# Kernel optimization log

Hardware: AMD Instinct MI355X
Metric: run time of the kernel (lower is better)

The kernel has to match this reference:

```python
import math
import jax, jax.numpy as jnp
import numpy as np


def setup_inputs() -> dict:
    key = jax.random.key(0)
    k1, k2 = jax.random.split(key)
    x = jax.random.normal(k1, (16, 256, 4096), dtype=jnp.float32)          # [B, D, T]
    codebooks = jax.random.normal(k2, (8, 1024, 256), dtype=jnp.float32)   # [n_q, bins, D]
    return {"x": x, "codebooks": codebooks, "sample_rate": 24000}


def _rvq(xt, codebooks):
    """Residual VQ on channels-last input xt: [B, T, D]. codebooks: [n_q, bins, D]."""
    n_q = codebooks.shape[0]
    residual = xt
    quant_out = jnp.zeros_like(xt)
    codes = []
    losses = []
    for i in range(n_q):
        cb = codebooks[i]                                   # [bins, D]
        # squared euclidean distance: ||r||^2 - 2 r.e + ||e||^2  -> [B, T, bins]
        dist = (jnp.sum(residual * residual, axis=-1, keepdims=True)
                - 2.0 * jnp.einsum("btd,kd->btk", residual, cb)
                + jnp.sum(cb * cb, axis=-1))
        idx = jnp.argmin(dist, axis=-1)                     # [B, T]
        q = cb[idx]                                         # gather -> [B, T, D]
        # straight-through estimator
        q_st = residual + jax.lax.stop_gradient(q - residual)
        # commitment loss: mse(stop_grad(quantize), residual)
        losses.append(jnp.mean((jax.lax.stop_gradient(q_st) - residual) ** 2))
        residual = residual - q_st
        quant_out = quant_out + q_st
        codes.append(idx)
    codes = jnp.stack(codes)                                # [n_q, B, T]
    commit_loss = jnp.stack(losses)                         # [n_q]
    return quant_out, codes, commit_loss


def reference(x, codebooks, sample_rate):
    n_q, bins, _ = codebooks.shape
    bw_per_q = math.log2(bins) * sample_rate / 1000.0
    xt = jnp.transpose(x, (0, 2, 1))                        # [B, T, D]
    quant_out, codes, commit_loss = _rvq(xt, codebooks)
    quantized = jnp.transpose(quant_out, (0, 2, 1))         # [B, D, T]
    bw = jnp.asarray(n_q * bw_per_q, dtype=x.dtype)
    return quantized, codes, bw, jnp.mean(commit_loss)
```

## Files before the change

### kernel.cpp

```cpp
#include <hip/hip_runtime.h>

#define B 16
#define D 256
#define T 4096
#define NQ 8
#define BINS 1024
#define EPS 0.008f

#define OFF_C  ((size_t)B * D * T)
#define OFF_BW (OFF_C + (size_t)NQ * B * T)
#define OFF_L  (OFF_BW + 1)

typedef __attribute__((ext_vector_type(8))) short short8v;
typedef __attribute__((ext_vector_type(4))) float float4v;

#define BBUF   0
#define RESF   0
#define IDXS   32768
#define FLAGS  33024
#define G1L    33280
#define RSTG   33536
#define NORMS  34560
#define REDW   38656
#define REDIW  38688
#define SMTOT  38704

#define STAGE16(gp, loff) \
  __builtin_amdgcn_global_load_lds( \
      (const __attribute__((address_space(1))) unsigned int*)(gp), \
      (__attribute__((address_space(3))) unsigned int*)(smc + (loff)), 16, 0, 0)

__device__ __forceinline__ unsigned short f2bf(float f) {
    unsigned u = __float_as_uint(f);
    unsigned r = (u + 0x7fffu + ((u >> 16) & 1u)) >> 16;
    return (unsigned short)r;
}
__device__ __forceinline__ float bf2f(unsigned short h) {
    return __uint_as_float(((unsigned)h) << 16);
}

__global__ __launch_bounds__(256) void cbnorm_kernel(const float* __restrict__ cb,
                                                     double* __restrict__ cbn,
                                                     float* __restrict__ cbnf)
{
    const int wave = threadIdx.x >> 6;
    const int lane = threadIdx.x & 63;
    const int bin = blockIdx.x * 4 + wave;
    const float4 v = *(const float4*)&cb[(size_t)bin * D + lane * 4];
    double a = (double)v.x * v.x + (double)v.y * v.y
             + (double)v.z * v.z + (double)v.w * v.w;
    #pragma unroll
    for (int off = 32; off >= 1; off >>= 1)
        a += __shfl_xor(a, off, 64);
    if (lane == 0) { cbn[bin] = a; cbnf[bin] = (float)a; }
}

__global__ __launch_bounds__(256) void prep_bfrag(const float* __restrict__ cb,
                                                  unsigned short* __restrict__ bfh,
                                                  unsigned short* __restrict__ bfl)
{
    const int c = blockIdx.x * 4 + (threadIdx.x >> 6);
    const int lane = threadIdx.x & 63;
    const int q = c >> 9, ntg = (c >> 3) & 63, ks = c & 7;
    const float* src = cb + ((size_t)q * BINS + ntg * 16 + (lane & 15)) * D
                         + ks * 32 + (lane >> 4) * 8;
    short8v h, l;
    #pragma unroll
    for (int j = 0; j < 8; ++j) {
        const float v = src[j];
        const unsigned short hh = f2bf(v);
        h[j] = (short)hh;
        l[j] = (short)f2bf(v - bf2f(hh));
    }
    const size_t off = ((size_t)c * 64 + lane) * 8;
    *(short8v*)(bfh + off) = h;
    *(short8v*)(bfl + off) = l;
}

__global__ __launch_bounds__(256, 4) void rvq_scan(
    const float* __restrict__ rsrc, float* __restrict__ rdst,
    const float* __restrict__ cb,
    const double* __restrict__ cbn, const float* __restrict__ cbnf,
    const unsigned short* __restrict__ bfh, const unsigned short* __restrict__ bfl,
    float* __restrict__ out, double* __restrict__ lpart, int q)
{
    __shared__ __align__(16) char smem[SMTOT];
    char*   smc    = smem;
    float*  resf   = (float*)(smem + RESF);
    int*    idxsL  = (int*)(smem + IDXS);
    int*    flagsL = (int*)(smem + FLAGS);
    float*  g1L    = (float*)(smem + G1L);
    float*  rstage = (float*)(smem + RSTG);
    float*  normsp = (float*)(smem + NORMS);
    double* redw   = (double*)(smem + REDW);
    int*    rediw  = (int*)(smem + REDIW);

    const int tid  = threadIdx.x;
    const int bid  = blockIdx.x;
    const int b    = bid >> 6;
    const int t0   = (bid & 63) * 64;
    const int w    = tid >> 6;
    const int lane = tid & 63;
    const int col  = lane & 15;
    const int rgrp = lane >> 4;
    const int rot  = (bid * 5) & 63;

    const float* rs = rsrc + (size_t)b * D * T + t0;
    float*       rd = rdst + (size_t)b * D * T + t0;

    for (int i = tid; i < BINS; i += 256) normsp[i] = cbnf[q * BINS + i];

    short8v Ah[8], Al[8];
    #pragma unroll 1
    for (int ch = 0; ch < 4; ++ch) {
        #pragma unroll 1
        for (int it = 0; it < 16; ++it) {
            const int lin = it * 256 + tid;
            const int tk = lin & 15, d = lin >> 4;
            resf[tk * 257 + d] = rs[(size_t)d * T + ch * 16 + tk];
        }
        __syncthreads();
        if (w == ch) {
            #pragma unroll
            for (int ks = 0; ks < 8; ++ks) {
                short8v h, l;
                #pragma unroll
                for (int j = 0; j < 8; ++j) {
                    const float v = resf[col * 257 + ks * 32 + rgrp * 8 + j];
                    const unsigned short hh = f2bf(v);
                    h[j] = (short)hh;
                    l[j] = (short)f2bf(v - bf2f(hh));
                }
                Ah[ks] = h; Al[ks] = l;
            }
        }
        __syncthreads();
    }

    const int plane = w >> 1, part = w & 1;
    const unsigned short* sbase = plane ? bfl : bfh;

    {
        const unsigned short* srcp =
            sbase + ((size_t)q * 512 + rot * 8 + part * 4) * 512 + lane * 8;
        const int dstb = plane * 8192 + part * 4096;
        #pragma unroll
        for (int i = 0; i < 4; ++i) STAGE16(srcp + i * 512, dstb + i * 1024);
    }

    float bv1[4], bv2[4]; int bi1[4];
    #pragma unroll
    for (int s = 0; s < 4; ++s) { bv1[s] = 3.4e38f; bv2[s] = 3.4e38f; bi1[s] = 0; }

    #pragma unroll 1
    for (int nt = 0; nt < 64; ++nt) {
        asm volatile("s_waitcnt vmcnt(0)" ::: "memory");
        __builtin_amdgcn_s_barrier();
        asm volatile("" ::: "memory");

        const int cur = nt & 1;
        if (nt < 63) {
            const int ntg = (nt + 1 + rot) & 63;
            const unsigned short* srcp =
                sbase + ((size_t)q * 512 + ntg * 8 + part * 4) * 512 + lane * 8;
            const int dstb = (cur ^ 1) * 16384 + plane * 8192 + part * 4096;
            #pragma unroll
            for (int i = 0; i < 4; ++i) STAGE16(srcp + i * 512, dstb + i * 1024);
        }
        asm volatile("" ::: "memory");

        const int ntr = (nt + rot) & 63;
        const char* bb = smc + cur * 16384;
        const float qn = normsp[ntr * 16 + col];

        float4v a0 = {0,0,0,0}, a1 = {0,0,0,0}, a2 = {0,0,0,0}, a3 = {0,0,0,0};
        __builtin_amdgcn_s_setprio(1);
        #pragma unroll
        for (int ks = 0; ks < 8; ++ks) {
            const short8v Bh = *(const short8v*)(bb + ks * 1024 + lane * 16);
            const short8v Bl = *(const short8v*)(bb + 8192 + ks * 1024 + lane * 16);
            float4v& c = (ks & 3) == 0 ? a0 : ((ks & 3) == 1 ? a1 : ((ks & 3) == 2 ? a2 : a3));
            c = __builtin_amdgcn_mfma_f32_16x16x32_bf16(Al[ks], Bh, c, 0, 0, 0);
            c = __builtin_amdgcn_mfma_f32_16x16x32_bf16(Ah[ks], Bl, c, 0, 0, 0);
            c = __builtin_amdgcn_mfma_f32_16x16x32_bf16(Ah[ks], Bh, c, 0, 0, 0);
        }
        __builtin_amdgcn_s_setprio(0);

        const int binb = ntr * 16 + col;
        #pragma unroll
        for (int r = 0; r < 4; ++r) {
            const float s0 = fmaf(-2.0f, (a0[r] + a1[r]) + (a2[r] + a3[r]), qn);
            if (s0 < bv1[r]) { bv2[r] = bv1[r]; bv1[r] = s0; bi1[r] = binb; }
            else if (s0 < bv2[r]) bv2[r] = s0;
        }
    }

    #pragma unroll
    for (int off = 1; off <= 8; off <<= 1) {
        #pragma unroll
        for (int sl = 0; sl < 4; ++sl) {
            const float ov1 = __shfl_xor(bv1[sl], off, 64);
            const float ov2 = __shfl_xor(bv2[sl], off, 64);
            const int   oi  = __shfl_xor(bi1[sl], off, 64);
            if (ov1 < bv1[sl] || (ov1 == bv1[sl] && oi < bi1[sl])) {
                bv2[sl] = fminf(bv1[sl], ov2); bv1[sl] = ov1; bi1[sl] = oi;
            } else {
                bv2[sl] = fminf(bv2[sl], ov1);
            }
        }
    }
    if (col == 0) {
        #pragma unroll
        for (int r = 0; r < 4; ++r) {
            const int tk = w * 16 + rgrp * 4 + r;
            idxsL[tk]  = bi1[r];
            g1L[tk]    = bv1[r];
            flagsL[tk] = (bv2[r] - bv1[r] < EPS) ? 1 : 0;
        }
    }
    __syncthreads();

    const float* cbq = cb + (size_t)q * BINS * D;
    #pragma unroll 1
    for (int tk2 = 0; tk2 < 64; ++tk2) {
        if (!flagsL[tk2]) continue;
        rstage[tid] = rs[(size_t)tid * T + tk2];
        __syncthreads();
        const float thr = g1L[tk2] + 0.0065f;
        double bb2 = 1e300; int bbi = 0x7fffffff;
        #pragma unroll 1
        for (int jj = 0; jj < 4; ++jj) {
            const int bin = tid + 256 * jj;
            const float* crow = cbq + (size_t)bin * D;
            float f0 = 0.f, f1 = 0.f, f2 = 0.f, f3 = 0.f;
            for (int d = 0; d < D; d += 4) {
                const float4 rv = *(const float4*)&rstage[d];
                const float4 cv = *(const float4*)&crow[d];
                f0 = fmaf(rv.x, cv.x, f0); f1 = fmaf(rv.y, cv.y, f1);
                f2 = fmaf(rv.z, cv.z, f2); f3 = fmaf(rv.w, cv.w, f3);
            }
            const float sf = fmaf(-2.0f, (f0 + f1) + (f2 + f3), normsp[bin]);
            if (sf <= thr) {
                double a = 0.0;
                for (int d = 0; d < D; d += 4) {
                    const float4 rv = *(const float4*)&rstage[d];
                    const float4 cv = *(const float4*)&crow[d];
                    a = fma((double)rv.x, (double)cv.x, a);
                    a = fma((double)rv.y, (double)cv.y, a);
                    a = fma((double)rv.z, (double)cv.z, a);
                    a = fma((double)rv.w, (double)cv.w, a);
                }
                const double s = fma(-2.0, a, cbn[q * BINS + bin]);
                if (s < bb2) { bb2 = s; bbi = bin; }
            }
        }
        #pragma unroll
        for (int off = 32; off >= 1; off >>= 1) {
            const double ov = __shfl_xor(bb2, off, 64);
            const int   oi  = __shfl_xor(bbi, off, 64);
            if (ov < bb2 || (ov == bb2 && oi < bbi)) { bb2 = ov; bbi = oi; }
        }
        if (lane == 0) { redw[w] = bb2; rediw[w] = bbi; }
        __syncthreads();
        if (tid == 0) {
            double mv = redw[0]; int mi = rediw[0];
            #pragma unroll
            for (int wv = 1; wv < 4; ++wv) {
                const double ov = redw[wv]; const int oi = rediw[wv];
                if (ov < mv || (ov == mv && oi < mi)) { mv = ov; mi = oi; }
            }
            idxsL[tk2] = mi;
        }
        __syncthreads();
    }

    if (tid < 64)
        out[OFF_C + (size_t)q * B * T + (size_t)b * T + t0 + tid] = (float)idxsL[tid];

    float* rows = resf;
    double lacc = 0.0;
    #pragma unroll 1
    for (int g = 0; g < 4; ++g) {
        __syncthreads();
        {
            const int j = tid >> 4, c = tid & 15;
            const float* crow = cbq + (size_t)idxsL[g * 16 + j] * D + c * 16;
            #pragma unroll
            for (int k2 = 0; k2 < 4; ++k2) {
                const float4 v = *(const float4*)(crow + k2 * 4);
                *(float4*)&rows[j * 257 + c * 16 + k2 * 4] = v;
            }
        }
        __syncthreads();
        #pragma unroll
        for (int it = 0; it < 16; ++it) {
            const int tk16 = tid & 15;
            const int dd_  = it * 16 + (tid >> 4);
            const int tk   = g * 16 + tk16;
            const float r  = rs[(size_t)dd_ * T + tk];
            const float cv = rows[tk16 * 257 + dd_];
            const float e   = cv - r;
            const float qst = r + e;
            const float dv  = qst - r;
            lacc = fma((double)dv, (double)dv, lacc);
            rd[(size_t)dd_ * T + tk] = r - qst;
        }
    }

    #pragma unroll
    for (int off = 32; off >= 1; off >>= 1)
        lacc += __shfl_xor(lacc, off, 64);
    __syncthreads();
    if (lane == 0) redw[w] = lacc;
    __syncthreads();
    if (tid == 0)
        lpart[(size_t)q * 1024 + bid] = (redw[0] + redw[1]) + (redw[2] + redw[3]);
}

__global__ __launch_bounds__(256) void final_sub(const float* __restrict__ x,
                                                 float* __restrict__ o)
{
    const size_t i = ((size_t)blockIdx.x * 256 + threadIdx.x) * 4;
    const float4v xv = __builtin_nontemporal_load((const float4v*)(x + i));
    const float4v ov = __builtin_nontemporal_load((const float4v*)(o + i));
    const float4v r = xv - ov;
    __builtin_nontemporal_store(r, (float4v*)(o + i));
}

#define OTOK 32
#define ORS 260
__global__ __launch_bounds__(256, 3) void rvq_main_old(
    const float* __restrict__ x, const float* __restrict__ cb,
    const double* __restrict__ cbn, const float* __restrict__ cbnf,
    float* __restrict__ out, double* __restrict__ lpart)
{
    __shared__ float  res[OTOK][ORS];
    __shared__ float  bv1s[OTOK][16];
    __shared__ float  bv2s[OTOK][16];
    __shared__ int    bi1s[OTOK][16];
    __shared__ int    idxs[OTOK];
    __shared__ int    flags[OTOK];
    __shared__ double fbv[256];
    __shared__ int    fbi[256];

    const int tid = threadIdx.x;
    const int bid = blockIdx.x;
    const int b  = bid >> 7;
    const int t0 = (bid & 127) * OTOK;

    const float* xb = x + (size_t)b * D * T + t0;
    #pragma unroll
    for (int it = 0; it < 32; ++it) {
        const int d  = it * 8 + (tid >> 5);
        const int tk = tid & 31;
        res[tk][d] = xb[(size_t)d * T + tk];
    }
    __syncthreads();

    float qreg[32];
    #pragma unroll
    for (int i = 0; i < 32; ++i) qreg[i] = 0.0f;

    const int tg = tid & 15;
    const int bg = tid >> 4;
    const int tku = tid >> 3;
    const int d0u = (tid & 7) * 32;
    double lacc = 0.0;

    for (int q = 0; q < NQ; ++q) {
        const float*  cbq = cb   + (size_t)q * BINS * D;
        const float*  cnf = cbnf + (size_t)q * BINS;
        const double* cnd = cbn  + (size_t)q * BINS;

        float bvA = 3.4e38f, bvA2 = 3.4e38f;  int biA = 0;
        float bvB = 3.4e38f, bvB2 = 3.4e38f;  int biB = 0;

        for (int iter = 0; iter < 8; ++iter) {
            const int binbase = iter * 128 + bg * 8;
            float a0[8], a1[8];
            #pragma unroll
            for (int j = 0; j < 8; ++j) { a0[j] = 0.0f; a1[j] = 0.0f; }
            for (int d = 0; d < D; d += 4) {
                const float4 r0 = *(const float4*)&res[tg][d];
                const float4 r1 = *(const float4*)&res[tg + 16][d];
                #pragma unroll
                for (int j = 0; j < 8; ++j) {
                    const float4 c = *(const float4*)&cbq[(size_t)(binbase + j) * D + d];
                    a0[j] = fmaf(r0.x, c.x, a0[j]); a0[j] = fmaf(r0.y, c.y, a0[j]);
                    a0[j] = fmaf(r0.z, c.z, a0[j]); a0[j] = fmaf(r0.w, c.w, a0[j]);
                    a1[j] = fmaf(r1.x, c.x, a1[j]); a1[j] = fmaf(r1.y, c.y, a1[j]);
                    a1[j] = fmaf(r1.z, c.z, a1[j]); a1[j] = fmaf(r1.w, c.w, a1[j]);
                }
            }
            #pragma unroll
            for (int j = 0; j < 8; ++j) {
                const int bin = binbase + j;
                const float qn = cnf[bin];
                const float s0 = fmaf(-2.0f, a0[j], qn);
                const float s1 = fmaf(-2.0f, a1[j], qn);
                if (s0 < bvA) { bvA2 = bvA; bvA = s0; biA = bin; }
                else if (s0 < bvA2) { bvA2 = s0; }
                if (s1 < bvB) { bvB2 = bvB; bvB = s1; biB = bin; }
                else if (s1 < bvB2) { bvB2 = s1; }
            }
        }
        bv1s[tg][bg]      = bvA;  bv2s[tg][bg]      = bvA2;  bi1s[tg][bg]      = biA;
        bv1s[tg + 16][bg] = bvB;  bv2s[tg + 16][bg] = bvB2;  bi1s[tg + 16][bg] = biB;
        __syncthreads();

        if (tid < OTOK) {
            float g1 = bv1s[tid][0], g2 = bv2s[tid][0];
            int   gi = bi1s[tid][0];
            #pragma unroll
            for (int g = 1; g < 16; ++g) {
                const float v1 = bv1s[tid][g];
                const float v2 = bv2s[tid][g];
                const int   i1 = bi1s[tid][g];
                if (v1 < g1 || (v1 == g1 && i1 < gi)) { g2 = fminf(g1, v2); g1 = v1; gi = i1; }
                else g2 = fminf(g2, v1);
            }
            idxs[tid]  = gi;
            flags[tid] = (g2 - g1 < 0.02f) ? 1 : 0;
        }
        __syncthreads();

        for (int tok = 0; tok < OTOK; ++tok) {
            if (!flags[tok]) continue;
            double bb = 1e300; int bbi = 0;
            #pragma unroll
            for (int jj = 0; jj < 4; ++jj) {
                const int bin = tid + 256 * jj;
                const float* crow = cbq + (size_t)bin * D;
                double a = 0.0;
                for (int d = 0; d < D; d += 4) {
                    const float4 r = *(const float4*)&res[tok][d];
                    const float4 c = *(const float4*)&crow[d];
                    a = fma((double)r.x, (double)c.x, a);
                    a = fma((double)r.y, (double)c.y, a);
                    a = fma((double)r.z, (double)c.z, a);
                    a = fma((double)r.w, (double)c.w, a);
                }
                const double s = fma(-2.0, a, cnd[bin]);
                if (s < bb) { bb = s; bbi = bin; }
            }
            fbv[tid] = bb; fbi[tid] = bbi;
            __syncthreads();
            for (int s2 = 128; s2 >= 1; s2 >>= 1) {
                if (tid < s2) {
                    const double ov = fbv[tid + s2]; const int oi = fbi[tid + s2];
                    const double mv = fbv[tid];      const int mi = fbi[tid];
                    if (ov < mv || (ov == mv && oi < mi)) { fbv[tid] = ov; fbi[tid] = oi; }
                }
                __syncthreads();
            }
            if (tid == 0) idxs[tok] = fbi[0];
            __syncthreads();
        }

        if (tid < OTOK)
            out[OFF_C + (size_t)q * B * T + (size_t)b * T + t0 + tid] = (float)idxs[tid];

        const float* crow = cbq + (size_t)idxs[tku] * D;
        #pragma unroll
        for (int i = 0; i < 8; ++i) {
            const int d = d0u + i * 4;
            const float4 qv = *(const float4*)&crow[d];
            float4 r = *(float4*)&res[tku][d];
            float e, qst, dd;
            e = qv.x - r.x; qst = r.x + e; dd = qst - r.x;
            lacc = fma((double)dd, (double)dd, lacc); qreg[i*4+0] += qst; r.x = r.x - qst;
            e = qv.y - r.y; qst = r.y + e; dd = qst - r.y;
            lacc = fma((double)dd, (double)dd, lacc); qreg[i*4+1] += qst; r.y = r.y - qst;
            e = qv.z - r.z; qst = r.z + e; dd = qst - r.z;
            lacc = fma((double)dd, (double)dd, lacc); qreg[i*4+2] += qst; r.z = r.z - qst;
            e = qv.w - r.w; qst = r.w + e; dd = qst - r.w;
            lacc = fma((double)dd, (double)dd, lacc); qreg[i*4+3] += qst; r.w = r.w - qst;
            *(float4*)&res[tku][d] = r;
        }
        __syncthreads();
    }

    #pragma unroll
    for (int i = 0; i < 8; ++i)
        *(float4*)&res[tku][d0u + i * 4] = *(float4*)&qreg[i * 4];
    __syncthreads();
    #pragma unroll
    for (int it = 0; it < 32; ++it) {
        const int d  = it * 8 + (tid >> 5);
        const int tk = tid & 31;
        out[(size_t)b * D * T + (size_t)d * T + t0 + tk] = res[tk][d];
    }

    fbv[tid] = lacc;
    __syncthreads();
    for (int s2 = 128; s2 >= 1; s2 >>= 1) {
        if (tid < s2) fbv[tid] += fbv[tid + s2];
        __syncthreads();
    }
    if (tid == 0) lpart[bid] = fbv[0];
}

__global__ __launch_bounds__(256) void finalize_kernel(
    const double* __restrict__ lpart, int nblk,
    const int* __restrict__ srp, float* __restrict__ out)
{
    __shared__ double sh[256];
    double a = 0.0;
    for (int i = threadIdx.x; i < nblk; i += 256) a += lpart[i];
    sh[threadIdx.x] = a;
    __syncthreads();
    for (int s = 128; s >= 1; s >>= 1) {
        if (threadIdx.x < s) sh[threadIdx.x] += sh[threadIdx.x + s];
        __syncthreads();
    }
    if (threadIdx.x == 0) {
        out[OFF_L]  = (float)(sh[0] / ((double)NQ * B * T * D));
        out[OFF_BW] = (float)((double)NQ * 10.0 * (double)srp[0] / 1000.0);
    }
}

extern "C" void kernel_launch(void* const* d_in, const int* in_sizes, int n_in,
                              void* d_out, int out_size, void* d_ws, size_t ws_size,
                              hipStream_t stream)
{
    const float* x  = (const float*)d_in[0];
    const float* cb = (const float*)d_in[1];
    const int*   sr = (const int*)d_in[2];
    float* out = (float*)d_out;

    double* cbn   = (double*)d_ws;
    float*  cbnf  = (float*)((char*)d_ws + 65536);
    double* lpart = (double*)((char*)d_ws + 98304);
    unsigned short* bfh = (unsigned short*)((char*)d_ws + 163840);
    unsigned short* bfl = (unsigned short*)((char*)d_ws + 4358144);

    hipLaunchKernelGGL(cbnorm_kernel, dim3(NQ * BINS / 4), dim3(256), 0, stream, cb, cbn, cbnf);

    if (ws_size >= (size_t)8552448) {
        hipLaunchKernelGGL(prep_bfrag, dim3(1024), dim3(256), 0, stream, cb, bfh, bfl);
        float* resb = out;
        for (int q = 0; q < NQ; ++q) {
            hipLaunchKernelGGL(rvq_scan, dim3(B * (T / 64)), dim3(256), 0, stream,
                               (q == 0 ? x : (const float*)resb), resb, cb, cbn, cbnf,
                               bfh, bfl, out, lpart, q);
        }
        hipLaunchKernelGGL(final_sub, dim3((B * D * T) / 1024), dim3(256), 0, stream, x, resb);
        hipLaunchKernelGGL(finalize_kernel, dim3(1), dim3(256), 0, stream,
                           lpart, NQ * 1024, sr, out);
    } else {
        hipLaunchKernelGGL(rvq_main_old, dim3(B * (T / OTOK)), dim3(256), 0, stream,
                           x, cb, cbn, cbnf, out, lpart);
        hipLaunchKernelGGL(finalize_kernel, dim3(1), dim3(256), 0, stream,
                           lpart, B * (T / OTOK), sr, out);
    }
}
```

Measured before the change: 1.652 ms.

## Split codebook across wave pairs and give each wave two row tiles

Each wave now holds the bf16 hi/lo fragments for two 16-row tiles of residual vectors and scans only half of the codebook bins. Two waves sharing a row group split the bins between them, and their top-two candidates are merged through shared memory afterwards. Every codebook fragment read from LDS now feeds twice as many MFMAs, which halves the LDS reads per MFMA and halves the scan loop trip count. In exchange the kernel uses more registers and doubles the LDS staging buffer, so launch bounds drop to 2 blocks per CU and occupancy falls.

```diff
diff --git a/kernel.cpp b/kernel.cpp
--- a/kernel.cpp
+++ b/kernel.cpp
@@ -16,14 +16,17 @@
 
 #define BBUF   0
 #define RESF   0
-#define IDXS   32768
-#define FLAGS  33024
-#define G1L    33280
-#define RSTG   33536
-#define NORMS  34560
-#define REDW   38656
-#define REDIW  38688
-#define SMTOT  38704
+#define NORMS  65536
+#define MG1    69632
+#define MG2    70144
+#define MGI    70656
+#define IDXS   71168
+#define FLAGS  71424
+#define G1L    71680
+#define RSTG   71936
+#define REDW   72960
+#define REDIW  72992
+#define SMTOT  73008
 
 #define STAGE16(gp, loff) \
   __builtin_amdgcn_global_load_lds( \
@@ -77,7 +80,7 @@
     *(short8v*)(bfl + off) = l;
 }
 
-__global__ __launch_bounds__(256, 4) void rvq_scan(
+__global__ __launch_bounds__(256, 2) void rvq_scan(
     const float* __restrict__ rsrc, float* __restrict__ rdst,
     const float* __restrict__ cb,
     const double* __restrict__ cbn, const float* __restrict__ cbnf,
@@ -87,11 +90,14 @@
     __shared__ __align__(16) char smem[SMTOT];
     char*   smc    = smem;
     float*  resf   = (float*)(smem + RESF);
+    float*  normsp = (float*)(smem + NORMS);
+    float*  mg1    = (float*)(smem + MG1);
+    float*  mg2    = (float*)(smem + MG2);
+    int*    mgi    = (int*)(smem + MGI);
     int*    idxsL  = (int*)(smem + IDXS);
     int*    flagsL = (int*)(smem + FLAGS);
     float*  g1L    = (float*)(smem + G1L);
     float*  rstage = (float*)(smem + RSTG);
-    float*  normsp = (float*)(smem + NORMS);
     double* redw   = (double*)(smem + REDW);
     int*    rediw  = (int*)(smem + REDIW);
 
@@ -103,14 +109,16 @@
     const int lane = tid & 63;
     const int col  = lane & 15;
     const int rgrp = lane >> 4;
-    const int rot  = (bid * 5) & 63;
+    const int tg   = w >> 1;
+    const int bh   = w & 1;
+    const int rot  = (bid * 5) & 31;
 
     const float* rs = rsrc + (size_t)b * D * T + t0;
     float*       rd = rdst + (size_t)b * D * T + t0;
 
     for (int i = tid; i < BINS; i += 256) normsp[i] = cbnf[q * BINS + i];
 
-    short8v Ah[8], Al[8];
+    short8v Ah0[8], Al0[8], Ah1[8], Al1[8];
     #pragma unroll 1
     for (int ch = 0; ch < 4; ++ch) {
         #pragma unroll 1
@@ -120,7 +128,8 @@
             resf[tk * 257 + d] = rs[(size_t)d * T + ch * 16 + tk];
         }
         __syncthreads();
-        if (w == ch) {
+        if ((ch >> 1) == tg) {
+            const int mt = ch & 1;
             #pragma unroll
             for (int ks = 0; ks < 8; ++ks) {
                 short8v h, l;
@@ -131,74 +140,83 @@
                     h[j] = (short)hh;
                     l[j] = (short)f2bf(v - bf2f(hh));
                 }
-                Ah[ks] = h; Al[ks] = l;
-            }
-        }
-        __syncthreads();
-    }
-
-    const int plane = w >> 1, part = w & 1;
-    const unsigned short* sbase = plane ? bfl : bfh;
+                if (mt == 0) { Ah0[ks] = h; Al0[ks] = l; }
+                else         { Ah1[ks] = h; Al1[ks] = l; }
+            }
+        }
+        __syncthreads();
+    }
+
+    const int sh = w & 1, sp = w >> 1;
+    const unsigned short* sbase = sp ? bfl : bfh;
 
     {
         const unsigned short* srcp =
-            sbase + ((size_t)q * 512 + rot * 8 + part * 4) * 512 + lane * 8;
-        const int dstb = plane * 8192 + part * 4096;
-        #pragma unroll
-        for (int i = 0; i < 4; ++i) STAGE16(srcp + i * 512, dstb + i * 1024);
-    }
-
-    float bv1[4], bv2[4]; int bi1[4];
-    #pragma unroll
-    for (int s = 0; s < 4; ++s) { bv1[s] = 3.4e38f; bv2[s] = 3.4e38f; bi1[s] = 0; }
+            sbase + ((size_t)q * 512 + (sh * 32 + rot) * 8) * 512 + lane * 8;
+        const int dstb = sh * 16384 + sp * 8192;
+        #pragma unroll
+        for (int i = 0; i < 8; ++i) STAGE16(srcp + i * 512, dstb + i * 1024);
+    }
+
+    float bv1[8], bv2[8]; int bi1[8];
+    #pragma unroll
+    for (int s = 0; s < 8; ++s) { bv1[s] = 3.4e38f; bv2[s] = 3.4e38f; bi1[s] = 0; }
 
     #pragma unroll 1
-    for (int nt = 0; nt < 64; ++nt) {
+    for (int nt = 0; nt < 32; ++nt) {
         asm volatile("s_waitcnt vmcnt(0)" ::: "memory");
         __builtin_amdgcn_s_barrier();
         asm volatile("" ::: "memory");
 
         const int cur = nt & 1;
-        if (nt < 63) {
-            const int ntg = (nt + 1 + rot) & 63;
+        if (nt < 31) {
+            const int ntg = (nt + 1 + rot) & 31;
             const unsigned short* srcp =
-                sbase + ((size_t)q * 512 + ntg * 8 + part * 4) * 512 + lane * 8;
-            const int dstb = (cur ^ 1) * 16384 + plane * 8192 + part * 4096;
-            #pragma unroll
-            for (int i = 0; i < 4; ++i) STAGE16(srcp + i * 512, dstb + i * 1024);
+                sbase + ((size_t)q * 512 + (sh * 32 + ntg) * 8) * 512 + lane * 8;
+            const int dstb = (cur ^ 1) * 32768 + sh * 16384 + sp * 8192;
+            #pragma unroll
+            for (int i = 0; i < 8; ++i) STAGE16(srcp + i * 512, dstb + i * 1024);
         }
         asm volatile("" ::: "memory");
 
-        const int ntr = (nt + rot) & 63;
-        const char* bb = smc + cur * 16384;
-        const float qn = normsp[ntr * 16 + col];
-
-        float4v a0 = {0,0,0,0}, a1 = {0,0,0,0}, a2 = {0,0,0,0}, a3 = {0,0,0,0};
+        const int ntr = (nt + rot) & 31;
+        const char* bbse = smc + cur * 32768 + bh * 16384;
+        const int binb = bh * 512 + ntr * 16 + col;
+        const float qn = normsp[binb];
+
+        float4v a00 = {0,0,0,0}, a01 = {0,0,0,0}, a02 = {0,0,0,0}, a03 = {0,0,0,0};
+        float4v a10 = {0,0,0,0}, a11 = {0,0,0,0}, a12 = {0,0,0,0}, a13 = {0,0,0,0};
         __builtin_amdgcn_s_setprio(1);
         #pragma unroll
         for (int ks = 0; ks < 8; ++ks) {
-            const short8v Bh = *(const short8v*)(bb + ks * 1024 + lane * 16);
-            const short8v Bl = *(const short8v*)(bb + 8192 + ks * 1024 + lane * 16);
-            float4v& c = (ks & 3) == 0 ? a0 : ((ks & 3) == 1 ? a1 : ((ks & 3) == 2 ? a2 : a3));
-            c = __builtin_amdgcn_mfma_f32_16x16x32_bf16(Al[ks], Bh, c, 0, 0, 0);
-            c = __builtin_amdgcn_mfma_f32_16x16x32_bf16(Ah[ks], Bl, c, 0, 0, 0);
-            c = __builtin_amdgcn_mfma_f32_16x16x32_bf16(Ah[ks], Bh, c, 0, 0, 0);
+            const short8v Bh = *(const short8v*)(bbse + ks * 1024 + lane * 16);
+            const short8v Bl = *(const short8v*)(bbse + 8192 + ks * 1024 + lane * 16);
+            float4v& c0 = (ks & 3) == 0 ? a00 : ((ks & 3) == 1 ? a01 : ((ks & 3) == 2 ? a02 : a03));
+            float4v& c1 = (ks & 3) == 0 ? a10 : ((ks & 3) == 1 ? a11 : ((ks & 3) == 2 ? a12 : a13));
+            c0 = __builtin_amdgcn_mfma_f32_16x16x32_bf16(Al0[ks], Bh, c0, 0, 0, 0);
+            c1 = __builtin_amdgcn_mfma_f32_16x16x32_bf16(Al1[ks], Bh, c1, 0, 0, 0);
+            c0 = __builtin_amdgcn_mfma_f32_16x16x32_bf16(Ah0[ks], Bl, c0, 0, 0, 0);
+            c1 = __builtin_amdgcn_mfma_f32_16x16x32_bf16(Ah1[ks], Bl, c1, 0, 0, 0);
+            c0 = __builtin_amdgcn_mfma_f32_16x16x32_bf16(Ah0[ks], Bh, c0, 0, 0, 0);
+            c1 = __builtin_amdgcn_mfma_f32_16x16x32_bf16(Ah1[ks], Bh, c1, 0, 0, 0);
         }
         __builtin_amdgcn_s_setprio(0);
 
-        const int binb = ntr * 16 + col;
         #pragma unroll
         for (int r = 0; r < 4; ++r) {
-            const float s0 = fmaf(-2.0f, (a0[r] + a1[r]) + (a2[r] + a3[r]), qn);
+            const float s0 = fmaf(-2.0f, (a00[r] + a01[r]) + (a02[r] + a03[r]), qn);
             if (s0 < bv1[r]) { bv2[r] = bv1[r]; bv1[r] = s0; bi1[r] = binb; }
             else if (s0 < bv2[r]) bv2[r] = s0;
+            const float s1 = fmaf(-2.0f, (a10[r] + a11[r]) + (a12[r] + a13[r]), qn);
+            if (s1 < bv1[4+r]) { bv2[4+r] = bv1[4+r]; bv1[4+r] = s1; bi1[4+r] = binb; }
+            else if (s1 < bv2[4+r]) bv2[4+r] = s1;
         }
     }
 
     #pragma unroll
     for (int off = 1; off <= 8; off <<= 1) {
         #pragma unroll
-        for (int sl = 0; sl < 4; ++sl) {
+        for (int sl = 0; sl < 8; ++sl) {
             const float ov1 = __shfl_xor(bv1[sl], off, 64);
             const float ov2 = __shfl_xor(bv2[sl], off, 64);
             const int   oi  = __shfl_xor(bi1[sl], off, 64);
@@ -211,12 +229,27 @@
     }
     if (col == 0) {
         #pragma unroll
-        for (int r = 0; r < 4; ++r) {
-            const int tk = w * 16 + rgrp * 4 + r;
-            idxsL[tk]  = bi1[r];
-            g1L[tk]    = bv1[r];
-            flagsL[tk] = (bv2[r] - bv1[r] < EPS) ? 1 : 0;
-        }
+        for (int mt = 0; mt < 2; ++mt)
+            #pragma unroll
+            for (int r = 0; r < 4; ++r) {
+                const int tk = tg * 32 + mt * 16 + rgrp * 4 + r;
+                const int sl = mt * 4 + r;
+                mg1[tk * 2 + bh] = bv1[sl];
+                mg2[tk * 2 + bh] = bv2[sl];
+                mgi[tk * 2 + bh] = bi1[sl];
+            }
+    }
+    __syncthreads();
+
+    if (tid < 64) {
+        float g1 = mg1[tid*2], g2 = mg2[tid*2]; int gi = mgi[tid*2];
+        const float v1 = mg1[tid*2+1], v2 = mg2[tid*2+1];
+        const int   i1 = mgi[tid*2+1];
+        if (v1 < g1 || (v1 == g1 && i1 < gi)) { g2 = fminf(g1, v2); g1 = v1; gi = i1; }
+        else g2 = fminf(g2, v1);
+        idxsL[tid]  = gi;
+        g1L[tid]    = g1;
+        flagsL[tid] = (g2 - g1 < EPS) ? 1 : 0;
     }
     __syncthreads();
 
```

New measurement: 2.013 ms. +21.8%, slower.
